# Performance work log

Measured on AMD Instinct MI355X. Metric: run time of the kernel, lower is better.

The kernel has to match this reference:

```python
import jax, jax.numpy as jnp
import numpy as np

B, S, D, V = 4, 512, 512, 32000
GAMMA = 0.5
EPS = 1e-12  # torch F.normalize clamp_min eps


def _l2norm(x, axis):
    n = jnp.sqrt(jnp.sum(x * x, axis=axis, keepdims=True))
    return x / jnp.maximum(n, EPS)


def setup_inputs() -> dict:
    key = jax.random.key(0)
    k1, k2, k3 = jax.random.split(key, 3)
    preds = jax.random.normal(k1, (B, D, S), dtype=jnp.float32)
    emb_weight = jax.random.normal(k2, (V, D), dtype=jnp.float32)
    target = jax.random.randint(k3, (B, S), 0, V, dtype=jnp.int64)
    return {"preds": preds, "emb_weight": emb_weight, "target": target, "pad_id": 0}


def reference(preds, emb_weight, target, pad_id):
    # preds: [B, D, S] -> [B, S, D], L2-normalized over D
    out_norm = _l2norm(jnp.transpose(preds, (0, 2, 1)), axis=2)
    voc_norm = _l2norm(emb_weight, axis=1)          # [V, D]
    tgt_emb = emb_weight[target]                     # [B, S, D] (raw lookup, not normalized)
    mask = target != pad_id                          # [B, S]

    cos_out_voc = jnp.einsum('bsd,vd->bsv', out_norm, voc_norm)  # [B, S, V]
    tgt_voc = jnp.einsum('bsd,vd->bsv', tgt_emb, voc_norm)       # [B, S, V]

    jmax = jnp.argmax(cos_out_voc - tgt_voc, axis=2)             # [B, S]
    cos_target = jnp.take_along_axis(cos_out_voc, target[..., None], axis=2)[..., 0]
    max_cos_voc = jnp.take_along_axis(cos_out_voc, jmax[..., None], axis=2)[..., 0]

    diff = jnp.maximum(GAMMA + max_cos_voc - cos_target, 0.0)    # [B, S]
    denom = jnp.sum(mask).astype(diff.dtype)
    return jnp.sum(jnp.where(mask, diff, 0.0)) / denom
```

## Files before the change

### kernel.cpp

```cpp
#include <hip/hip_runtime.h>
#include <math.h>


#define Bb 4
#define Ss 512
#define Dd 512
#define Vv 32000
#define ROWS (Bb * Ss)
#define NTILE_M (ROWS / 128)
#define NTILE_N (Vv / 128)

typedef __attribute__((ext_vector_type(8))) short bf16x8;
typedef __attribute__((ext_vector_type(4))) float f32x4;

__device__ __forceinline__ float waveReduceSum(float x) {
#pragma unroll
  for (int m = 32; m >= 1; m >>= 1) x += __shfl_xor(x, m, 64);
  return x;
}

__device__ __forceinline__ unsigned short f2bf(float f) {
  unsigned u = __float_as_uint(f);
  unsigned r = (u + 0x7FFFu + ((u >> 16) & 1u)) >> 16;
  return (unsigned short)r;
}

__device__ __forceinline__ unsigned long long packSC(float s, int c) {
  unsigned b = __float_as_uint(s);
  unsigned key = b ^ ((b & 0x80000000u) ? 0xFFFFFFFFu : 0x80000000u);
  return ((unsigned long long)key << 32) | (unsigned)(~c);
}

__device__ __forceinline__ void async_ld16(const void* g, void* l) {
  __builtin_amdgcn_global_load_lds((const __attribute__((address_space(1))) void*)g,
                                   (__attribute__((address_space(3))) void*)l, 16, 0, 0);
}

__global__ __launch_bounds__(256) void prep_rows(
    const float* __restrict__ preds, const float* __restrict__ emb,
    const int* __restrict__ target,
    float* __restrict__ o_rows, short* __restrict__ u_bf,
    float* __restrict__ cos_tgt) {
  int row = blockIdx.x;
  int b = row >> 9, s = row & (Ss - 1);
  int tid = threadIdx.x;
  int wave = tid >> 6, lane = tid & 63;
  const float* p = preds + (size_t)b * Dd * Ss + s;
  float x0 = p[(size_t)tid * Ss];
  float x1 = p[(size_t)(tid + 256) * Ss];
  __shared__ float red[12];
  float ss = waveReduceSum(x0 * x0 + x1 * x1);
  if (lane == 0) red[wave] = ss;
  __syncthreads();
  float inv = 1.0f / fmaxf(sqrtf(red[0] + red[1] + red[2] + red[3]), 1e-12f);
  float o0 = x0 * inv, o1 = x1 * inv;
  o_rows[(size_t)row * Dd + tid] = o0;
  o_rows[(size_t)row * Dd + tid + 256] = o1;
  int t = target[row];
  const float* et = emb + (size_t)t * Dd;
  float e0 = et[tid], e1 = et[tid + 256];
  u_bf[(size_t)row * Dd + tid] = (short)f2bf(o0 - e0);
  u_bf[(size_t)row * Dd + tid + 256] = (short)f2bf(o1 - e1);
  float ss2 = waveReduceSum(e0 * e0 + e1 * e1);
  float dt = waveReduceSum(o0 * e0 + o1 * e1);
  if (lane == 0) { red[4 + wave] = ss2; red[8 + wave] = dt; }
  __syncthreads();
  if (tid == 0) {
    float n2 = red[4] + red[5] + red[6] + red[7];
    float dd = red[8] + red[9] + red[10] + red[11];
    cos_tgt[row] = dd * (1.0f / fmaxf(sqrtf(n2), 1e-12f));
  }
}

__global__ __launch_bounds__(256) void voc_prep(const float* __restrict__ emb,
                                                short* __restrict__ ebf,
                                                float* __restrict__ inv_norm) {
  int v = blockIdx.x * 4 + (threadIdx.x >> 6);
  int lane = threadIdx.x & 63;
  const float* e = emb + (size_t)v * Dd;
  float4 x0 = *(const float4*)(e + lane * 8);
  float4 x1 = *(const float4*)(e + lane * 8 + 4);
  float ss = x0.x * x0.x + x0.y * x0.y + x0.z * x0.z + x0.w * x0.w +
             x1.x * x1.x + x1.y * x1.y + x1.z * x1.z + x1.w * x1.w;
  ss = waveReduceSum(ss);
  float inv = 1.0f / fmaxf(sqrtf(ss), 1e-12f);
  bf16x8 o;
  o[0] = (short)f2bf(x0.x * inv); o[1] = (short)f2bf(x0.y * inv);
  o[2] = (short)f2bf(x0.z * inv); o[3] = (short)f2bf(x0.w * inv);
  o[4] = (short)f2bf(x1.x * inv); o[5] = (short)f2bf(x1.y * inv);
  o[6] = (short)f2bf(x1.z * inv); o[7] = (short)f2bf(x1.w * inv);
  *(bf16x8*)(ebf + (size_t)v * Dd + lane * 8) = o;
  if (lane == 0) inv_norm[v] = inv;
}

__global__ __launch_bounds__(256) void gemm_argmax(
    const short* __restrict__ u_bf, const short* __restrict__ ebf,
    unsigned long long* __restrict__ part) {
  __shared__ short sA[128 * 32];
  __shared__ short sB[128 * 32];
  int tm = blockIdx.x, tn = blockIdx.y;
  int tid = threadIdx.x;
  int w = tid >> 6, lane = tid & 63;
  int wm = w >> 1, wn = w & 1;

  const short* gA = u_bf + ((size_t)(tm * 128 + w * 32 + (lane >> 2)) * Dd) + (lane & 3) * 8;
  const short* gB = ebf + ((size_t)(tn * 128 + w * 32 + (lane >> 2)) * Dd) + (lane & 3) * 8;
  short* lA = &sA[(w * 32) * 32];
  short* lB = &sB[(w * 32) * 32];

  const short* pa = &sA[(lane & 15) * 32 + (lane >> 4) * 8];
  const short* pb = &sB[(lane & 15) * 32 + (lane >> 4) * 8];

  f32x4 acc[4][4];
  f32x4 z = {0.f, 0.f, 0.f, 0.f};
#pragma unroll
  for (int mi = 0; mi < 4; ++mi)
#pragma unroll
    for (int ni = 0; ni < 4; ++ni) acc[mi][ni] = z;

  for (int kk = 0; kk < Dd / 32; ++kk) {
    __syncthreads();
    async_ld16(gA + kk * 32, lA);
    async_ld16(gA + 16 * Dd + kk * 32, lA + 16 * 32);
    async_ld16(gB + kk * 32, lB);
    async_ld16(gB + 16 * Dd + kk * 32, lB + 16 * 32);
    __syncthreads();
    bf16x8 af[4], bg[4];
#pragma unroll
    for (int mi = 0; mi < 4; ++mi)
      af[mi] = *(const bf16x8*)(pa + (wm * 64 + mi * 16) * 32);
#pragma unroll
    for (int ni = 0; ni < 4; ++ni)
      bg[ni] = *(const bf16x8*)(pb + (wn * 64 + ni * 16) * 32);
#pragma unroll
    for (int mi = 0; mi < 4; ++mi)
#pragma unroll
      for (int ni = 0; ni < 4; ++ni)
        acc[mi][ni] = __builtin_amdgcn_mfma_f32_16x16x32_bf16(af[mi], bg[ni], acc[mi][ni], 0, 0, 0);
  }

  float bs[4][4];
  int bc[4][4];
  int col0 = tn * 128 + wn * 64 + (lane & 15);
#pragma unroll
  for (int mi = 0; mi < 4; ++mi) {
#pragma unroll
    for (int j = 0; j < 4; ++j) { bs[mi][j] = acc[mi][0][j]; bc[mi][j] = col0; }
#pragma unroll
    for (int ni = 1; ni < 4; ++ni) {
      int c = col0 + ni * 16;
#pragma unroll
      for (int j = 0; j < 4; ++j) {
        float v = acc[mi][ni][j];
        if (v > bs[mi][j]) { bs[mi][j] = v; bc[mi][j] = c; }
      }
    }
  }
#pragma unroll
  for (int m = 1; m < 16; m <<= 1) {
#pragma unroll
    for (int mi = 0; mi < 4; ++mi)
#pragma unroll
      for (int j = 0; j < 4; ++j) {
        float os = __shfl_xor(bs[mi][j], m, 64);
        int oc = __shfl_xor(bc[mi][j], m, 64);
        if (os > bs[mi][j] || (os == bs[mi][j] && oc < bc[mi][j])) {
          bs[mi][j] = os;
          bc[mi][j] = oc;
        }
      }
  }
  __syncthreads();
  float* sEs = (float*)sA;
  int* sEc = (int*)sA + 256;
  if ((lane & 15) == 0) {
    int q = lane >> 4;
#pragma unroll
    for (int mi = 0; mi < 4; ++mi)
#pragma unroll
      for (int j = 0; j < 4; ++j) {
        int rloc = wm * 64 + mi * 16 + q * 4 + j;
        sEs[wn * 128 + rloc] = bs[mi][j];
        sEc[wn * 128 + rloc] = bc[mi][j];
      }
  }
  __syncthreads();
  if (tid < 128) {
    float s0 = sEs[tid], s1 = sEs[128 + tid];
    int c0 = sEc[tid], c1 = sEc[128 + tid];
    if (s1 > s0 || (s1 == s0 && c1 < c0)) { s0 = s1; c0 = c1; }
    part[(size_t)tn * ROWS + tm * 128 + tid] = packSC(s0, c0);
  }
}

__global__ __launch_bounds__(256) void row_final(
    const float* __restrict__ o_rows, const float* __restrict__ emb,
    const float* __restrict__ inv_norm, const float* __restrict__ cos_tgt,
    const int* __restrict__ target, const int* __restrict__ pad_id,
    const unsigned long long* __restrict__ part, float* __restrict__ diffs) {
  int wave = threadIdx.x >> 6, lane = threadIdx.x & 63;
  int row = blockIdx.x * 4 + wave;
  unsigned long long best = 0ull;
  for (int t = lane; t < NTILE_N; t += 64) {
    unsigned long long p = part[(size_t)t * ROWS + row];
    if (p > best) best = p;
  }
#pragma unroll
  for (int m = 1; m < 64; m <<= 1) {
    unsigned long long o = __shfl_xor(best, m, 64);
    if (o > best) best = o;
  }
  int bi = (int)(~(unsigned)(best & 0xFFFFFFFFull));
  const float* o = o_rows + (size_t)row * Dd;
  const float* e = emb + (size_t)bi * Dd;
  float d = 0.f;
#pragma unroll
  for (int i = 0; i < Dd / 64; ++i) d += o[lane + 64 * i] * e[lane + 64 * i];
  d = waveReduceSum(d);
  if (lane == 0) {
    float cmax = d * inv_norm[bi];
    int t = target[row];
    float df = fmaxf(0.5f + cmax - cos_tgt[row], 0.0f);
    diffs[row] = (t != pad_id[0]) ? df : 0.0f;
  }
}

__global__ __launch_bounds__(256) void reduce_final(
    const float* __restrict__ diffs, const int* __restrict__ target,
    const int* __restrict__ pad_id, float* __restrict__ out) {
  int tid = threadIdx.x;
  int pid = pad_id[0];
  float s = 0.f, c = 0.f;
  for (int i = tid; i < ROWS; i += 256) {
    s += diffs[i];
    c += (target[i] != pid) ? 1.0f : 0.0f;
  }
  s = waveReduceSum(s);
  c = waveReduceSum(c);
  __shared__ float rs[4], rc[4];
  int wave = tid >> 6, lane = tid & 63;
  if (lane == 0) { rs[wave] = s; rc[wave] = c; }
  __syncthreads();
  if (tid == 0) out[0] = (rs[0] + rs[1] + rs[2] + rs[3]) / (rc[0] + rc[1] + rc[2] + rc[3]);
}

extern "C" void kernel_launch(void* const* d_in, const int* in_sizes, int n_in,
                              void* d_out, int out_size, void* d_ws, size_t ws_size,
                              hipStream_t stream) {
  const float* preds = (const float*)d_in[0];
  const float* emb = (const float*)d_in[1];
  const int* target = (const int*)d_in[2];
  const int* pad_id = (const int*)d_in[3];
  char* ws = (char*)d_ws;
  float* o_rows = (float*)ws;
  short* u_bf = (short*)(ws + 4194304);
  short* ebf = (short*)(ws + 6291456);
  float* inv_norm = (float*)(ws + 39059456);
  float* cos_tgt = (float*)(ws + 39187456);
  unsigned long long* part = (unsigned long long*)(ws + 39195648);
  float* diffs = (float*)(ws + 43291648);

  prep_rows<<<ROWS, 256, 0, stream>>>(preds, emb, target, o_rows, u_bf, cos_tgt);
  voc_prep<<<Vv / 4, 256, 0, stream>>>(emb, ebf, inv_norm);
  dim3 g(NTILE_M, NTILE_N);
  gemm_argmax<<<g, 256, 0, stream>>>(u_bf, ebf, part);
  row_final<<<ROWS / 4, 256, 0, stream>>>(o_rows, emb, inv_norm, cos_tgt, target,
                                          pad_id, part, diffs);
  reduce_final<<<1, 256, 0, stream>>>(diffs, target, pad_id, (float*)d_out);
}
```

Measured before the change: 230.2 us.

## Load GEMM fragments directly from global into registers with register double-buffering

The gemm_argmax kernel no longer stages A/B tiles through LDS with async global_load_lds and two barriers per k-step. Each lane now loads its MFMA fragments straight from global memory into registers and double-buffers them (a0/b0, a1/b1) so the next k-slice's loads overlap the current MFMAs. Launch bounds also request 3 blocks per SM. This removes the per-iteration barriers and LDS traffic, but gives up cross-wave data sharing: each wave reloads the same rows as its neighbours (duplicate global/L2 traffic), uses more registers, and issues strided 16-byte loads.

```diff
diff --git a/kernel.cpp b/kernel.cpp
--- a/kernel.cpp
+++ b/kernel.cpp
@@ -29,11 +29,6 @@
   unsigned b = __float_as_uint(s);
   unsigned key = b ^ ((b & 0x80000000u) ? 0xFFFFFFFFu : 0x80000000u);
   return ((unsigned long long)key << 32) | (unsigned)(~c);
-}
-
-__device__ __forceinline__ void async_ld16(const void* g, void* l) {
-  __builtin_amdgcn_global_load_lds((const __attribute__((address_space(1))) void*)g,
-                                   (__attribute__((address_space(3))) void*)l, 16, 0, 0);
 }
 
 __global__ __launch_bounds__(256) void prep_rows(
@@ -93,23 +88,24 @@
   if (lane == 0) inv_norm[v] = inv;
 }
 
-__global__ __launch_bounds__(256) void gemm_argmax(
+__global__ __launch_bounds__(256, 3) void gemm_argmax(
     const short* __restrict__ u_bf, const short* __restrict__ ebf,
     unsigned long long* __restrict__ part) {
-  __shared__ short sA[128 * 32];
-  __shared__ short sB[128 * 32];
   int tm = blockIdx.x, tn = blockIdx.y;
   int tid = threadIdx.x;
   int w = tid >> 6, lane = tid & 63;
   int wm = w >> 1, wn = w & 1;
-
-  const short* gA = u_bf + ((size_t)(tm * 128 + w * 32 + (lane >> 2)) * Dd) + (lane & 3) * 8;
-  const short* gB = ebf + ((size_t)(tn * 128 + w * 32 + (lane >> 2)) * Dd) + (lane & 3) * 8;
-  short* lA = &sA[(w * 32) * 32];
-  short* lB = &sB[(w * 32) * 32];
-
-  const short* pa = &sA[(lane & 15) * 32 + (lane >> 4) * 8];
-  const short* pb = &sB[(lane & 15) * 32 + (lane >> 4) * 8];
+  int fr = lane & 15;
+  int kofs = (lane >> 4) * 8;
+
+  const bf16x8* pA[4];
+  const bf16x8* pB[4];
+#pragma unroll
+  for (int mi = 0; mi < 4; ++mi)
+    pA[mi] = (const bf16x8*)(u_bf + (size_t)(tm * 128 + wm * 64 + mi * 16 + fr) * Dd + kofs);
+#pragma unroll
+  for (int ni = 0; ni < 4; ++ni)
+    pB[ni] = (const bf16x8*)(ebf + (size_t)(tn * 128 + wn * 64 + ni * 16 + fr) * Dd + kofs);
 
   f32x4 acc[4][4];
   f32x4 z = {0.f, 0.f, 0.f, 0.f};
@@ -118,25 +114,36 @@
 #pragma unroll
     for (int ni = 0; ni < 4; ++ni) acc[mi][ni] = z;
 
-  for (int kk = 0; kk < Dd / 32; ++kk) {
-    __syncthreads();
-    async_ld16(gA + kk * 32, lA);
-    async_ld16(gA + 16 * Dd + kk * 32, lA + 16 * 32);
-    async_ld16(gB + kk * 32, lB);
-    async_ld16(gB + 16 * Dd + kk * 32, lB + 16 * 32);
-    __syncthreads();
-    bf16x8 af[4], bg[4];
-#pragma unroll
-    for (int mi = 0; mi < 4; ++mi)
-      af[mi] = *(const bf16x8*)(pa + (wm * 64 + mi * 16) * 32);
-#pragma unroll
-    for (int ni = 0; ni < 4; ++ni)
-      bg[ni] = *(const bf16x8*)(pb + (wn * 64 + ni * 16) * 32);
+  bf16x8 a0[4], b0[4], a1[4], b1[4];
+#pragma unroll
+  for (int mi = 0; mi < 4; ++mi) a0[mi] = pA[mi][0];
+#pragma unroll
+  for (int ni = 0; ni < 4; ++ni) b0[ni] = pB[ni][0];
+
+#pragma unroll
+  for (int kk = 0; kk < Dd / 32; kk += 2) {
+    if (kk + 1 < Dd / 32) {
+#pragma unroll
+      for (int mi = 0; mi < 4; ++mi) a1[mi] = pA[mi][(kk + 1) * 4];
+#pragma unroll
+      for (int ni = 0; ni < 4; ++ni) b1[ni] = pB[ni][(kk + 1) * 4];
+    }
 #pragma unroll
     for (int mi = 0; mi < 4; ++mi)
 #pragma unroll
       for (int ni = 0; ni < 4; ++ni)
-        acc[mi][ni] = __builtin_amdgcn_mfma_f32_16x16x32_bf16(af[mi], bg[ni], acc[mi][ni], 0, 0, 0);
+        acc[mi][ni] = __builtin_amdgcn_mfma_f32_16x16x32_bf16(a0[mi], b0[ni], acc[mi][ni], 0, 0, 0);
+    if (kk + 2 < Dd / 32) {
+#pragma unroll
+      for (int mi = 0; mi < 4; ++mi) a0[mi] = pA[mi][(kk + 2) * 4];
+#pragma unroll
+      for (int ni = 0; ni < 4; ++ni) b0[ni] = pB[ni][(kk + 2) * 4];
+    }
+#pragma unroll
+    for (int mi = 0; mi < 4; ++mi)
+#pragma unroll
+      for (int ni = 0; ni < 4; ++ni)
+        acc[mi][ni] = __builtin_amdgcn_mfma_f32_16x16x32_bf16(a1[mi], b1[ni], acc[mi][ni], 0, 0, 0);
   }
 
   float bs[4][4];
@@ -170,9 +177,8 @@
         }
       }
   }
-  __syncthreads();
-  float* sEs = (float*)sA;
-  int* sEc = (int*)sA + 256;
+  __shared__ float sEs[256];
+  __shared__ int sEc[256];
   if ((lane & 15) == 0) {
     int q = lane >> 4;
 #pragma unroll
```

Measured after the change: 367.7 us. 1.6x slower.

## Widen GEMM K-tile to 64 with XOR-swizzled LDS, XCD-aware block remap, batch prep rows

Applied to the files above, without the earlier changes.

The GEMM now stages 64-wide K slices in LDS, which halves the barrier-separated iterations and issues two MFMA sweeps per iteration. The LDS layout uses an XOR swizzle on the 16-byte chunks to avoid bank conflicts. Block IDs are remapped to a 1D grid so that blocks sharing a vocab tile land on the same XCD, improving L2 reuse. prep_rows handles four consecutive rows per block with float4 loads along S, making the strided transpose read coalesced. LDS use doubles and there is still no double buffering.

```diff
diff --git a/kernel.cpp b/kernel.cpp
--- a/kernel.cpp
+++ b/kernel.cpp
@@ -41,34 +41,52 @@
     const int* __restrict__ target,
     float* __restrict__ o_rows, short* __restrict__ u_bf,
     float* __restrict__ cos_tgt) {
-  int row = blockIdx.x;
-  int b = row >> 9, s = row & (Ss - 1);
+  int row0 = blockIdx.x * 4;
+  int b = row0 >> 9, s0 = row0 & (Ss - 1);
   int tid = threadIdx.x;
   int wave = tid >> 6, lane = tid & 63;
-  const float* p = preds + (size_t)b * Dd * Ss + s;
-  float x0 = p[(size_t)tid * Ss];
-  float x1 = p[(size_t)(tid + 256) * Ss];
-  __shared__ float red[12];
-  float ss = waveReduceSum(x0 * x0 + x1 * x1);
-  if (lane == 0) red[wave] = ss;
-  __syncthreads();
-  float inv = 1.0f / fmaxf(sqrtf(red[0] + red[1] + red[2] + red[3]), 1e-12f);
-  float o0 = x0 * inv, o1 = x1 * inv;
-  o_rows[(size_t)row * Dd + tid] = o0;
-  o_rows[(size_t)row * Dd + tid + 256] = o1;
-  int t = target[row];
-  const float* et = emb + (size_t)t * Dd;
-  float e0 = et[tid], e1 = et[tid + 256];
-  u_bf[(size_t)row * Dd + tid] = (short)f2bf(o0 - e0);
-  u_bf[(size_t)row * Dd + tid + 256] = (short)f2bf(o1 - e1);
-  float ss2 = waveReduceSum(e0 * e0 + e1 * e1);
-  float dt = waveReduceSum(o0 * e0 + o1 * e1);
-  if (lane == 0) { red[4 + wave] = ss2; red[8 + wave] = dt; }
-  __syncthreads();
-  if (tid == 0) {
-    float n2 = red[4] + red[5] + red[6] + red[7];
-    float dd = red[8] + red[9] + red[10] + red[11];
-    cos_tgt[row] = dd * (1.0f / fmaxf(sqrtf(n2), 1e-12f));
+  const float* p = preds + (size_t)b * Dd * Ss;
+  float4 x0 = *(const float4*)(p + (size_t)tid * Ss + s0);
+  float4 x1 = *(const float4*)(p + (size_t)(tid + 256) * Ss + s0);
+  float a0[4] = {x0.x, x0.y, x0.z, x0.w};
+  float a1[4] = {x1.x, x1.y, x1.z, x1.w};
+  __shared__ float rA[4][4], rB[4][4], rC[4][4];
+  float sq[4];
+#pragma unroll
+  for (int j = 0; j < 4; ++j) sq[j] = waveReduceSum(a0[j] * a0[j] + a1[j] * a1[j]);
+  if (lane == 0)
+#pragma unroll
+    for (int j = 0; j < 4; ++j) rA[wave][j] = sq[j];
+  __syncthreads();
+  float o0[4], o1[4];
+#pragma unroll
+  for (int j = 0; j < 4; ++j) {
+    float inv = 1.0f / fmaxf(sqrtf(rA[0][j] + rA[1][j] + rA[2][j] + rA[3][j]), 1e-12f);
+    o0[j] = a0[j] * inv;
+    o1[j] = a1[j] * inv;
+    o_rows[(size_t)(row0 + j) * Dd + tid] = o0[j];
+    o_rows[(size_t)(row0 + j) * Dd + tid + 256] = o1[j];
+  }
+  float ss2[4], dt[4];
+#pragma unroll
+  for (int j = 0; j < 4; ++j) {
+    int t = target[row0 + j];
+    const float* et = emb + (size_t)t * Dd;
+    float e0 = et[tid], e1 = et[tid + 256];
+    u_bf[(size_t)(row0 + j) * Dd + tid] = (short)f2bf(o0[j] - e0);
+    u_bf[(size_t)(row0 + j) * Dd + tid + 256] = (short)f2bf(o1[j] - e1);
+    ss2[j] = waveReduceSum(e0 * e0 + e1 * e1);
+    dt[j] = waveReduceSum(o0[j] * e0 + o1[j] * e1);
+  }
+  if (lane == 0)
+#pragma unroll
+    for (int j = 0; j < 4; ++j) { rB[wave][j] = ss2[j]; rC[wave][j] = dt[j]; }
+  __syncthreads();
+  if (tid < 4) {
+    int j = tid;
+    float n2 = rB[0][j] + rB[1][j] + rB[2][j] + rB[3][j];
+    float dd = rC[0][j] + rC[1][j] + rC[2][j] + rC[3][j];
+    cos_tgt[row0 + j] = dd * (1.0f / fmaxf(sqrtf(n2), 1e-12f));
   }
 }
 
@@ -96,20 +114,24 @@
 __global__ __launch_bounds__(256) void gemm_argmax(
     const short* __restrict__ u_bf, const short* __restrict__ ebf,
     unsigned long long* __restrict__ part) {
-  __shared__ short sA[128 * 32];
-  __shared__ short sB[128 * 32];
-  int tm = blockIdx.x, tn = blockIdx.y;
+  __shared__ short sA[128 * 64];
+  __shared__ short sB[128 * 64];
+  int bid = blockIdx.x;
+  int g = (bid & 7) * 500 + (bid >> 3);
+  int tm = g & 15, tn = g >> 4;
   int tid = threadIdx.x;
   int w = tid >> 6, lane = tid & 63;
   int wm = w >> 1, wn = w & 1;
 
-  const short* gA = u_bf + ((size_t)(tm * 128 + w * 32 + (lane >> 2)) * Dd) + (lane & 3) * 8;
-  const short* gB = ebf + ((size_t)(tn * 128 + w * 32 + (lane >> 2)) * Dd) + (lane & 3) * 8;
-  short* lA = &sA[(w * 32) * 32];
-  short* lB = &sB[(w * 32) * 32];
-
-  const short* pa = &sA[(lane & 15) * 32 + (lane >> 4) * 8];
-  const short* pb = &sB[(lane & 15) * 32 + (lane >> 4) * 8];
+  int srow = w * 8 + (lane >> 3);
+  int schunk = (lane & 7) ^ ((lane >> 3) & 7);
+  const short* gA = u_bf + (size_t)(tm * 128 + srow) * Dd + schunk * 8;
+  const short* gB = ebf + (size_t)(tn * 128 + srow) * Dd + schunk * 8;
+
+  int fr = lane & 15;
+  int q = lane >> 4;
+  int ck0 = ((q) ^ (fr & 7)) * 8;
+  int ck1 = ((4 + q) ^ (fr & 7)) * 8;
 
   f32x4 acc[4][4];
   f32x4 z = {0.f, 0.f, 0.f, 0.f};
@@ -118,25 +140,41 @@
 #pragma unroll
     for (int ni = 0; ni < 4; ++ni) acc[mi][ni] = z;
 
-  for (int kk = 0; kk < Dd / 32; ++kk) {
+  for (int kk = 0; kk < Dd / 64; ++kk) {
     __syncthreads();
-    async_ld16(gA + kk * 32, lA);
-    async_ld16(gA + 16 * Dd + kk * 32, lA + 16 * 32);
-    async_ld16(gB + kk * 32, lB);
-    async_ld16(gB + 16 * Dd + kk * 32, lB + 16 * 32);
+    {
+      const short* ga = gA + kk * 64;
+      const short* gb = gB + kk * 64;
+#pragma unroll
+      for (int i = 0; i < 4; ++i) {
+        async_ld16(ga + (size_t)(i * 32) * Dd, &sA[(w * 8 + i * 32) * 64]);
+        async_ld16(gb + (size_t)(i * 32) * Dd, &sB[(w * 8 + i * 32) * 64]);
+      }
+    }
     __syncthreads();
-    bf16x8 af[4], bg[4];
+    bf16x8 af0[4], af1[4], bg0[4], bg1[4];
+#pragma unroll
+    for (int mi = 0; mi < 4; ++mi) {
+      int r = (wm * 64 + mi * 16 + fr) * 64;
+      af0[mi] = *(const bf16x8*)(sA + r + ck0);
+      af1[mi] = *(const bf16x8*)(sA + r + ck1);
+    }
+#pragma unroll
+    for (int ni = 0; ni < 4; ++ni) {
+      int r = (wn * 64 + ni * 16 + fr) * 64;
+      bg0[ni] = *(const bf16x8*)(sB + r + ck0);
+      bg1[ni] = *(const bf16x8*)(sB + r + ck1);
+    }
 #pragma unroll
     for (int mi = 0; mi < 4; ++mi)
-      af[mi] = *(const bf16x8*)(pa + (wm * 64 + mi * 16) * 32);
-#pragma unroll
-    for (int ni = 0; ni < 4; ++ni)
-      bg[ni] = *(const bf16x8*)(pb + (wn * 64 + ni * 16) * 32);
+#pragma unroll
+      for (int ni = 0; ni < 4; ++ni)
+        acc[mi][ni] = __builtin_amdgcn_mfma_f32_16x16x32_bf16(af0[mi], bg0[ni], acc[mi][ni], 0, 0, 0);
 #pragma unroll
     for (int mi = 0; mi < 4; ++mi)
 #pragma unroll
       for (int ni = 0; ni < 4; ++ni)
-        acc[mi][ni] = __builtin_amdgcn_mfma_f32_16x16x32_bf16(af[mi], bg[ni], acc[mi][ni], 0, 0, 0);
+        acc[mi][ni] = __builtin_amdgcn_mfma_f32_16x16x32_bf16(af1[mi], bg1[ni], acc[mi][ni], 0, 0, 0);
   }
 
   float bs[4][4];
@@ -174,12 +212,12 @@
   float* sEs = (float*)sA;
   int* sEc = (int*)sA + 256;
   if ((lane & 15) == 0) {
-    int q = lane >> 4;
+    int qq = lane >> 4;
 #pragma unroll
     for (int mi = 0; mi < 4; ++mi)
 #pragma unroll
       for (int j = 0; j < 4; ++j) {
-        int rloc = wm * 64 + mi * 16 + q * 4 + j;
+        int rloc = wm * 64 + mi * 16 + qq * 4 + j;
         sEs[wn * 128 + rloc] = bs[mi][j];
         sEc[wn * 128 + rloc] = bc[mi][j];
       }
@@ -260,10 +298,9 @@
   unsigned long long* part = (unsigned long long*)(ws + 39195648);
   float* diffs = (float*)(ws + 43291648);
 
-  prep_rows<<<ROWS, 256, 0, stream>>>(preds, emb, target, o_rows, u_bf, cos_tgt);
+  prep_rows<<<ROWS / 4, 256, 0, stream>>>(preds, emb, target, o_rows, u_bf, cos_tgt);
   voc_prep<<<Vv / 4, 256, 0, stream>>>(emb, ebf, inv_norm);
-  dim3 g(NTILE_M, NTILE_N);
-  gemm_argmax<<<g, 256, 0, stream>>>(u_bf, ebf, part);
+  gemm_argmax<<<NTILE_M * NTILE_N, 256, 0, stream>>>(u_bf, ebf, part);
   row_final<<<ROWS / 4, 256, 0, stream>>>(o_rows, emb, inv_norm, cos_tgt, target,
                                           pad_id, part, diffs);
   reduce_final<<<1, 256, 0, stream>>>(diffs, target, pad_id, (float*)d_out);
```

New measurement: 220.0 us. -4.4%, faster.

## Fuse prep kernels, double K-tile with swizzled LDS, remap GEMM block order

Applied to the files above, without the earlier changes.

Merges the row and vocabulary prep kernels into one launch so a kernel boundary and its tail idle time go away. In the GEMM, the K step grows from 32 to 64 per barrier pair, which halves the synchronisations. The LDS layout uses an XOR chunk swizzle to avoid bank conflicts. A 1D grid with a remapped block index is meant to improve L2 reuse across the tile assignment, and launch bounds request 4 blocks per CU. The cost is twice the LDS per block and a more complex index mapping.

```diff
diff --git a/kernel.cpp b/kernel.cpp
--- a/kernel.cpp
+++ b/kernel.cpp
@@ -9,6 +9,7 @@
 #define ROWS (Bb * Ss)
 #define NTILE_M (ROWS / 128)
 #define NTILE_N (Vv / 128)
+#define VOC_BLOCKS (Vv / 4)
 
 typedef __attribute__((ext_vector_type(8))) short bf16x8;
 typedef __attribute__((ext_vector_type(4))) float f32x4;
@@ -36,80 +37,82 @@
                                    (__attribute__((address_space(3))) void*)l, 16, 0, 0);
 }
 
-__global__ __launch_bounds__(256) void prep_rows(
+__global__ __launch_bounds__(256) void prep_all(
     const float* __restrict__ preds, const float* __restrict__ emb,
     const int* __restrict__ target,
     float* __restrict__ o_rows, short* __restrict__ u_bf,
-    float* __restrict__ cos_tgt) {
-  int row = blockIdx.x;
-  int b = row >> 9, s = row & (Ss - 1);
+    float* __restrict__ cos_tgt, short* __restrict__ ebf,
+    float* __restrict__ inv_norm) {
   int tid = threadIdx.x;
   int wave = tid >> 6, lane = tid & 63;
-  const float* p = preds + (size_t)b * Dd * Ss + s;
-  float x0 = p[(size_t)tid * Ss];
-  float x1 = p[(size_t)(tid + 256) * Ss];
-  __shared__ float red[12];
-  float ss = waveReduceSum(x0 * x0 + x1 * x1);
-  if (lane == 0) red[wave] = ss;
-  __syncthreads();
-  float inv = 1.0f / fmaxf(sqrtf(red[0] + red[1] + red[2] + red[3]), 1e-12f);
-  float o0 = x0 * inv, o1 = x1 * inv;
-  o_rows[(size_t)row * Dd + tid] = o0;
-  o_rows[(size_t)row * Dd + tid + 256] = o1;
-  int t = target[row];
-  const float* et = emb + (size_t)t * Dd;
-  float e0 = et[tid], e1 = et[tid + 256];
-  u_bf[(size_t)row * Dd + tid] = (short)f2bf(o0 - e0);
-  u_bf[(size_t)row * Dd + tid + 256] = (short)f2bf(o1 - e1);
-  float ss2 = waveReduceSum(e0 * e0 + e1 * e1);
-  float dt = waveReduceSum(o0 * e0 + o1 * e1);
-  if (lane == 0) { red[4 + wave] = ss2; red[8 + wave] = dt; }
-  __syncthreads();
-  if (tid == 0) {
-    float n2 = red[4] + red[5] + red[6] + red[7];
-    float dd = red[8] + red[9] + red[10] + red[11];
-    cos_tgt[row] = dd * (1.0f / fmaxf(sqrtf(n2), 1e-12f));
-  }
-}
-
-__global__ __launch_bounds__(256) void voc_prep(const float* __restrict__ emb,
-                                                short* __restrict__ ebf,
-                                                float* __restrict__ inv_norm) {
-  int v = blockIdx.x * 4 + (threadIdx.x >> 6);
-  int lane = threadIdx.x & 63;
-  const float* e = emb + (size_t)v * Dd;
-  float4 x0 = *(const float4*)(e + lane * 8);
-  float4 x1 = *(const float4*)(e + lane * 8 + 4);
-  float ss = x0.x * x0.x + x0.y * x0.y + x0.z * x0.z + x0.w * x0.w +
-             x1.x * x1.x + x1.y * x1.y + x1.z * x1.z + x1.w * x1.w;
-  ss = waveReduceSum(ss);
-  float inv = 1.0f / fmaxf(sqrtf(ss), 1e-12f);
-  bf16x8 o;
-  o[0] = (short)f2bf(x0.x * inv); o[1] = (short)f2bf(x0.y * inv);
-  o[2] = (short)f2bf(x0.z * inv); o[3] = (short)f2bf(x0.w * inv);
-  o[4] = (short)f2bf(x1.x * inv); o[5] = (short)f2bf(x1.y * inv);
-  o[6] = (short)f2bf(x1.z * inv); o[7] = (short)f2bf(x1.w * inv);
-  *(bf16x8*)(ebf + (size_t)v * Dd + lane * 8) = o;
-  if (lane == 0) inv_norm[v] = inv;
-}
-
-__global__ __launch_bounds__(256) void gemm_argmax(
+  if (blockIdx.x < VOC_BLOCKS) {
+    int v = blockIdx.x * 4 + wave;
+    const float* e = emb + (size_t)v * Dd;
+    float4 x0 = *(const float4*)(e + lane * 8);
+    float4 x1 = *(const float4*)(e + lane * 8 + 4);
+    float ss = x0.x * x0.x + x0.y * x0.y + x0.z * x0.z + x0.w * x0.w +
+               x1.x * x1.x + x1.y * x1.y + x1.z * x1.z + x1.w * x1.w;
+    ss = waveReduceSum(ss);
+    float inv = 1.0f / fmaxf(sqrtf(ss), 1e-12f);
+    bf16x8 o;
+    o[0] = (short)f2bf(x0.x * inv); o[1] = (short)f2bf(x0.y * inv);
+    o[2] = (short)f2bf(x0.z * inv); o[3] = (short)f2bf(x0.w * inv);
+    o[4] = (short)f2bf(x1.x * inv); o[5] = (short)f2bf(x1.y * inv);
+    o[6] = (short)f2bf(x1.z * inv); o[7] = (short)f2bf(x1.w * inv);
+    *(bf16x8*)(ebf + (size_t)v * Dd + lane * 8) = o;
+    if (lane == 0) inv_norm[v] = inv;
+  } else {
+    int row = blockIdx.x - VOC_BLOCKS;
+    int b = row >> 9, s = row & (Ss - 1);
+    const float* p = preds + (size_t)b * Dd * Ss + s;
+    float x0 = p[(size_t)tid * Ss];
+    float x1 = p[(size_t)(tid + 256) * Ss];
+    __shared__ float red[12];
+    float ss = waveReduceSum(x0 * x0 + x1 * x1);
+    if (lane == 0) red[wave] = ss;
+    __syncthreads();
+    float inv = 1.0f / fmaxf(sqrtf(red[0] + red[1] + red[2] + red[3]), 1e-12f);
+    float o0 = x0 * inv, o1 = x1 * inv;
+    o_rows[(size_t)row * Dd + tid] = o0;
+    o_rows[(size_t)row * Dd + tid + 256] = o1;
+    int t = target[row];
+    const float* et = emb + (size_t)t * Dd;
+    float e0 = et[tid], e1 = et[tid + 256];
+    u_bf[(size_t)row * Dd + tid] = (short)f2bf(o0 - e0);
+    u_bf[(size_t)row * Dd + tid + 256] = (short)f2bf(o1 - e1);
+    float ss2 = waveReduceSum(e0 * e0 + e1 * e1);
+    float dt = waveReduceSum(o0 * e0 + o1 * e1);
+    if (lane == 0) { red[4 + wave] = ss2; red[8 + wave] = dt; }
+    __syncthreads();
+    if (tid == 0) {
+      float n2 = red[4] + red[5] + red[6] + red[7];
+      float dd = red[8] + red[9] + red[10] + red[11];
+      cos_tgt[row] = dd * (1.0f / fmaxf(sqrtf(n2), 1e-12f));
+    }
+  }
+}
+
+__global__ __launch_bounds__(256, 4) void gemm_argmax(
     const short* __restrict__ u_bf, const short* __restrict__ ebf,
     unsigned long long* __restrict__ part) {
-  __shared__ short sA[128 * 32];
-  __shared__ short sB[128 * 32];
-  int tm = blockIdx.x, tn = blockIdx.y;
+  __shared__ short sA[128 * 64];
+  __shared__ short sB[128 * 64];
+  int bid = blockIdx.x;
+  int g = (bid & 7) * 500 + (bid >> 3);
+  int tm = g & 15, tn = g >> 4;
   int tid = threadIdx.x;
   int w = tid >> 6, lane = tid & 63;
   int wm = w >> 1, wn = w & 1;
 
-  const short* gA = u_bf + ((size_t)(tm * 128 + w * 32 + (lane >> 2)) * Dd) + (lane & 3) * 8;
-  const short* gB = ebf + ((size_t)(tn * 128 + w * 32 + (lane >> 2)) * Dd) + (lane & 3) * 8;
-  short* lA = &sA[(w * 32) * 32];
-  short* lB = &sB[(w * 32) * 32];
-
-  const short* pa = &sA[(lane & 15) * 32 + (lane >> 4) * 8];
-  const short* pb = &sB[(lane & 15) * 32 + (lane >> 4) * 8];
+  int srow = w * 8 + (lane >> 3);
+  int schunk = (lane & 7) ^ ((lane >> 3) & 7);
+  const short* gA = u_bf + (size_t)(tm * 128 + srow) * Dd + schunk * 8;
+  const short* gB = ebf + (size_t)(tn * 128 + srow) * Dd + schunk * 8;
+
+  int fr = lane & 15;
+  int q = lane >> 4;
+  int ck0 = ((q) ^ (fr & 7)) * 8;
+  int ck1 = ((4 + q) ^ (fr & 7)) * 8;
 
   f32x4 acc[4][4];
   f32x4 z = {0.f, 0.f, 0.f, 0.f};
@@ -118,20 +121,36 @@
 #pragma unroll
     for (int ni = 0; ni < 4; ++ni) acc[mi][ni] = z;
 
-  for (int kk = 0; kk < Dd / 32; ++kk) {
-    __syncthreads();
-    async_ld16(gA + kk * 32, lA);
-    async_ld16(gA + 16 * Dd + kk * 32, lA + 16 * 32);
-    async_ld16(gB + kk * 32, lB);
-    async_ld16(gB + 16 * Dd + kk * 32, lB + 16 * 32);
+  for (int kk = 0; kk < Dd / 64; ++kk) {
+    __syncthreads();
+    {
+      const short* ga = gA + kk * 64;
+      const short* gb = gB + kk * 64;
+#pragma unroll
+      for (int i = 0; i < 4; ++i) {
+        async_ld16(ga + (size_t)(i * 32) * Dd, &sA[(w * 8 + i * 32) * 64]);
+        async_ld16(gb + (size_t)(i * 32) * Dd, &sB[(w * 8 + i * 32) * 64]);
+      }
+    }
     __syncthreads();
     bf16x8 af[4], bg[4];
 #pragma unroll
     for (int mi = 0; mi < 4; ++mi)
-      af[mi] = *(const bf16x8*)(pa + (wm * 64 + mi * 16) * 32);
+      af[mi] = *(const bf16x8*)(sA + (wm * 64 + mi * 16 + fr) * 64 + ck0);
 #pragma unroll
     for (int ni = 0; ni < 4; ++ni)
-      bg[ni] = *(const bf16x8*)(pb + (wn * 64 + ni * 16) * 32);
+      bg[ni] = *(const bf16x8*)(sB + (wn * 64 + ni * 16 + fr) * 64 + ck0);
+#pragma unroll
+    for (int mi = 0; mi < 4; ++mi)
+#pragma unroll
+      for (int ni = 0; ni < 4; ++ni)
+        acc[mi][ni] = __builtin_amdgcn_mfma_f32_16x16x32_bf16(af[mi], bg[ni], acc[mi][ni], 0, 0, 0);
+#pragma unroll
+    for (int mi = 0; mi < 4; ++mi)
+      af[mi] = *(const bf16x8*)(sA + (wm * 64 + mi * 16 + fr) * 64 + ck1);
+#pragma unroll
+    for (int ni = 0; ni < 4; ++ni)
+      bg[ni] = *(const bf16x8*)(sB + (wn * 64 + ni * 16 + fr) * 64 + ck1);
 #pragma unroll
     for (int mi = 0; mi < 4; ++mi)
 #pragma unroll
@@ -174,12 +193,12 @@
   float* sEs = (float*)sA;
   int* sEc = (int*)sA + 256;
   if ((lane & 15) == 0) {
-    int q = lane >> 4;
+    int qq = lane >> 4;
 #pragma unroll
     for (int mi = 0; mi < 4; ++mi)
 #pragma unroll
       for (int j = 0; j < 4; ++j) {
-        int rloc = wm * 64 + mi * 16 + q * 4 + j;
+        int rloc = wm * 64 + mi * 16 + qq * 4 + j;
         sEs[wn * 128 + rloc] = bs[mi][j];
         sEc[wn * 128 + rloc] = bc[mi][j];
       }
@@ -260,10 +279,9 @@
   unsigned long long* part = (unsigned long long*)(ws + 39195648);
   float* diffs = (float*)(ws + 43291648);
 
-  prep_rows<<<ROWS, 256, 0, stream>>>(preds, emb, target, o_rows, u_bf, cos_tgt);
-  voc_prep<<<Vv / 4, 256, 0, stream>>>(emb, ebf, inv_norm);
-  dim3 g(NTILE_M, NTILE_N);
-  gemm_argmax<<<g, 256, 0, stream>>>(u_bf, ebf, part);
+  prep_all<<<VOC_BLOCKS + ROWS, 256, 0, stream>>>(preds, emb, target, o_rows, u_bf,
+                                                  cos_tgt, ebf, inv_norm);
+  gemm_argmax<<<NTILE_M * NTILE_N, 256, 0, stream>>>(u_bf, ebf, part);
   row_final<<<ROWS / 4, 256, 0, stream>>>(o_rows, emb, inv_norm, cos_tgt, target,
                                           pad_id, part, diffs);
   reduce_final<<<1, 256, 0, stream>>>(diffs, target, pad_id, (float*)d_out);
```

Result: faster. 206.8 us (-10.2%).
